# Kernel tuning notes

Measured on AMD Instinct MI355X. Metric: run time of the kernel, lower is better.

Reference implementation:

```python
import jax, jax.numpy as jnp
import numpy as np

N = 50000      # nodes
E = 1_600_000  # edges
IN, H, H2, OUT = 256, 128, 64, 2
EPS = 1e-5     # BatchNorm eps


def setup_inputs() -> dict:
    key = jax.random.key(0)
    ks = jax.random.split(key, 18)
    inp = {
        "x": jax.random.normal(ks[0], (N, IN), dtype=jnp.float32),
        "edge_index": jax.random.randint(ks[1], (2, E), 0, N, dtype=jnp.int64),
        # GCNConv 1
        "W1": jax.random.normal(ks[2], (IN, H), dtype=jnp.float32) / np.sqrt(IN),
        "b1": jnp.zeros((H,), dtype=jnp.float32),
        "g1": jnp.ones((H,), dtype=jnp.float32),
        "be1": jnp.zeros((H,), dtype=jnp.float32),
        "m1": jax.random.normal(ks[3], (H,), dtype=jnp.float32) * 0.1,
        "v1": jax.random.uniform(ks[4], (H,), dtype=jnp.float32, minval=0.5, maxval=1.5),
        # GCNConv 2
        "W2": jax.random.normal(ks[5], (H, H2), dtype=jnp.float32) / np.sqrt(H),
        "b2": jnp.zeros((H2,), dtype=jnp.float32),
        "g2": jnp.ones((H2,), dtype=jnp.float32),
        "be2": jnp.zeros((H2,), dtype=jnp.float32),
        "m2": jax.random.normal(ks[6], (H2,), dtype=jnp.float32) * 0.1,
        "v2": jax.random.uniform(ks[7], (H2,), dtype=jnp.float32, minval=0.5, maxval=1.5),
        # final linear
        "Wl": jax.random.normal(ks[8], (H2, OUT), dtype=jnp.float32) / np.sqrt(H2),
        "bl": jnp.zeros((OUT,), dtype=jnp.float32),
    }
    return inp


def _gcn_conv(x, W, b, src, dst, n_nodes):
    # PyG GCNConv: linear transform, then symmetric-normalized aggregation
    # with self-loops (gcn_norm, improved=False, fill_value=1).
    xw = x @ W                                            # [N, H]
    ones = jnp.ones((src.shape[0],), dtype=x.dtype)
    deg = jax.ops.segment_sum(ones, dst, num_segments=n_nodes) + 1.0  # +1 self-loop
    dinv = jax.lax.rsqrt(deg)                             # deg^{-1/2}
    norm = dinv[src] * dinv[dst]                          # [E]
    msgs = xw[src] * norm[:, None]                        # [E, H] gather
    agg = jax.ops.segment_sum(msgs, dst, num_segments=n_nodes)  # scatter-add
    agg = agg + xw * (1.0 / deg)[:, None]                 # self-loop term
    return agg + b


def _bn_relu(x, gamma, beta, mean, var):
    # inference-mode BatchNorm1d + ReLU
    xhat = (x - mean) * jax.lax.rsqrt(var + EPS)
    return jax.nn.relu(xhat * gamma + beta)


def reference(x, edge_index, W1, b1, g1, be1, m1, v1,
              W2, b2, g2, be2, m2, v2, Wl, bl):
    src, dst = edge_index[0], edge_index[1]
    h = _gcn_conv(x, W1, b1, src, dst, N)
    h = _bn_relu(h, g1, be1, m1, v1)
    # dropout is identity in eval mode
    h = _gcn_conv(h, W2, b2, src, dst, N)
    h = _bn_relu(h, g2, be2, m2, v2)
    return h @ Wl + bl
```

## Files before the change

### kernel.cpp

```cpp
#include <hip/hip_runtime.h>

#define N_NODES 50000
#define N_EDGES 1600000
#define IN_F 256
#define H1_F 128
#define H2_F 64
#define OUT_F 2
#define BN_EPS 1e-5f

#define NBUK 782
#define BCAP 3584
#define CHUNK 4096
#define NCHUNK 391

typedef __attribute__((ext_vector_type(8))) short bf16x8;
typedef __attribute__((ext_vector_type(4))) float f32x4;
typedef __attribute__((ext_vector_type(4))) int   i32x4;
typedef __attribute__((ext_vector_type(4))) unsigned u32x4;

__device__ __forceinline__ unsigned short f2b(float f) {
    union { float f; unsigned u; } v; v.f = f;
    unsigned r = (v.u + 0x7FFFu + ((v.u >> 16) & 1u)) >> 16;
    return (unsigned short)r;
}
__device__ __forceinline__ float b2f(unsigned short b) {
    union { unsigned u; float f; } v; v.u = ((unsigned)b) << 16;
    return v.f;
}
__device__ __forceinline__ void add2(float& a0, float& a1, unsigned u) {
    union { unsigned u; float f; } lo, hi;
    lo.u = u << 16;
    hi.u = u & 0xFFFF0000u;
    a0 += lo.f; a1 += hi.f;
}

__launch_bounds__(256)
__global__ void chist_prep_kernel(const int* __restrict__ dst, int* __restrict__ h,
                                  int* __restrict__ tot, int* __restrict__ deg,
                                  const float* __restrict__ W1, const float* __restrict__ W2,
                                  unsigned short* __restrict__ w1t, unsigned short* __restrict__ w2t,
                                  const float* __restrict__ g1, const float* __restrict__ be1,
                                  const float* __restrict__ m1, const float* __restrict__ v1,
                                  const float* __restrict__ b1,
                                  const float* __restrict__ g2, const float* __restrict__ be2,
                                  const float* __restrict__ m2, const float* __restrict__ v2,
                                  const float* __restrict__ b2,
                                  float* __restrict__ sc1, float* __restrict__ sh1,
                                  float* __restrict__ sc2, float* __restrict__ sh2) {
    const int blk = blockIdx.x;
    const int t   = threadIdx.x;
    if (blk < NCHUNK) {
        __shared__ int lh[NBUK];
        const int c = blk;
        for (int i = t; i < NBUK; i += 256) lh[i] = 0;
        __syncthreads();
        const int e0 = c * CHUNK;
        const int e1 = min(e0 + CHUNK, N_EDGES);
        const i32x4* p = (const i32x4*)(dst + e0);
        const int n4 = (e1 - e0) >> 2;
        for (int i = t; i < n4; i += 256) {
            i32x4 d = __builtin_nontemporal_load(p + i);
            atomicAdd(&lh[d.x >> 6], 1);
            atomicAdd(&lh[d.y >> 6], 1);
            atomicAdd(&lh[d.z >> 6], 1);
            atomicAdd(&lh[d.w >> 6], 1);
            atomicAdd(&deg[d.x], 1);
            atomicAdd(&deg[d.y], 1);
            atomicAdd(&deg[d.z], 1);
            atomicAdd(&deg[d.w], 1);
        }
        __syncthreads();
        for (int i = t; i < NBUK; i += 256) {
            int v = lh[i];
            h[(size_t)i * NCHUNK + c] = v;
            if (v) atomicAdd(&tot[i], v);
        }
    } else {
        const int blk2 = blk - NCHUNK;
        if (blk2 < 128) {
            int i = blk2 * 256 + t;
            int n = i / IN_F, k = i % IN_F;
            w1t[i] = f2b(W1[(size_t)k * H1_F + n]);
        } else if (blk2 < 160) {
            int i = (blk2 - 128) * 256 + t;
            int n = i / H1_F, k = i % H1_F;
            w2t[i] = f2b(W2[(size_t)k * H2_F + n]);
        } else {
            if (t < H1_F) {
                float s = g1[t] * rsqrtf(v1[t] + BN_EPS);
                sc1[t] = s;
                sh1[t] = (b1[t] - m1[t]) * s + be1[t];
            } else if (t < H1_F + H2_F) {
                int f = t - H1_F;
                float s = g2[f] * rsqrtf(v2[f] + BN_EPS);
                sc2[f] = s;
                sh2[f] = (b2[f] - m2[f]) * s + be2[f];
            }
        }
    }
}

__launch_bounds__(256)
__global__ void scanoffs_kernel(const int* __restrict__ tot, int* __restrict__ boff,
                                int* __restrict__ h, int* __restrict__ rowptr,
                                const int* __restrict__ deg, float* __restrict__ dinv) {
    const int b = (blockIdx.x * blockDim.x + threadIdx.x) >> 6;
    if (b >= NBUK) return;
    const int lane = threadIdx.x & 63;

    const int node = b * 64 + lane;
    if (node < N_NODES) dinv[node] = rsqrtf((float)deg[node] + 1.0f);

    int acc = 0;
    for (int i = lane; i < NBUK; i += 64)
        if (i < b) acc += tot[i];
#pragma unroll
    for (int off = 1; off < 64; off <<= 1) acc += __shfl_xor(acc, off);
    if (lane == 0) boff[b] = acc;
    if (b == 0 && lane == 0) { boff[NBUK] = N_EDGES; rowptr[N_NODES] = N_EDGES; }

    int run = acc;
    int* row = h + (size_t)b * NCHUNK;
    for (int c0 = 0; c0 < NCHUNK; c0 += 64) {
        int idx = c0 + lane;
        int v = (idx < NCHUNK) ? row[idx] : 0;
        int s = v;
#pragma unroll
        for (int off = 1; off < 64; off <<= 1) {
            int t2 = __shfl_up(s, off);
            if (lane >= off) s += t2;
        }
        if (idx < NCHUNK) row[idx] = run + (s - v);
        run += __shfl(s, 63);
    }
}

__launch_bounds__(256)
__global__ void cscatter_gemm1_kernel(const int* __restrict__ src, const int* __restrict__ dst,
                                      const int* __restrict__ h, unsigned* __restrict__ bedges,
                                      const float* __restrict__ x, const unsigned short* __restrict__ BT,
                                      const float* __restrict__ dinv, unsigned short* __restrict__ C) {
    __shared__ int cur[NBUK];
    const int blk = blockIdx.x;
    if (blk < NCHUNK) {
        const int c = blk;
        for (int i = threadIdx.x; i < NBUK; i += 256) cur[i] = h[(size_t)i * NCHUNK + c];
        __syncthreads();
        const int e0 = c * CHUNK;
        const int e1 = min(e0 + CHUNK, N_EDGES);
        const i32x4* pd = (const i32x4*)(dst + e0);
        const i32x4* ps = (const i32x4*)(src + e0);
        const int n4 = (e1 - e0) >> 2;
        for (int i = threadIdx.x; i < n4; i += 256) {
            i32x4 d = __builtin_nontemporal_load(pd + i);
            i32x4 s = __builtin_nontemporal_load(ps + i);
            int slot;
            slot = atomicAdd(&cur[d.x >> 6], 1); bedges[slot] = (unsigned)s.x | ((unsigned)d.x << 16);
            slot = atomicAdd(&cur[d.y >> 6], 1); bedges[slot] = (unsigned)s.y | ((unsigned)d.y << 16);
            slot = atomicAdd(&cur[d.z >> 6], 1); bedges[slot] = (unsigned)s.z | ((unsigned)d.z << 16);
            slot = atomicAdd(&cur[d.w >> 6], 1); bedges[slot] = (unsigned)s.w | ((unsigned)d.w << 16);
        }
    } else {
        constexpr int KSTEPS = IN_F / 32;
        constexpr int NTILES = H1_F / 16;
        constexpr int K  = IN_F;
        constexpr int NF = H1_F;
        const int bid2 = blk - NCHUNK;
        const int wave = threadIdx.x >> 6;
        const int lane = threadIdx.x & 63;
        const int r0   = (bid2 * 4 + wave) * 16;
        const int m    = lane & 15;
        const int kb   = lane >> 4;

        int arow = r0 + m;
        if (arow >= N_NODES) arow = N_NODES - 1;

        f32x4 acc[NTILES];
#pragma unroll
        for (int nt = 0; nt < NTILES; ++nt) acc[nt] = (f32x4)(0.f);

#pragma unroll
        for (int ks = 0; ks < KSTEPS; ++ks) {
            const int k0 = ks * 32 + kb * 8;
            const float* af = x + (size_t)arow * K + k0;
            f32x4 lo = __builtin_nontemporal_load((const f32x4*)af);
            f32x4 hi = __builtin_nontemporal_load((const f32x4*)(af + 4));
            union { bf16x8 v; unsigned short u[8]; } pk;
            pk.u[0] = f2b(lo.x); pk.u[1] = f2b(lo.y); pk.u[2] = f2b(lo.z); pk.u[3] = f2b(lo.w);
            pk.u[4] = f2b(hi.x); pk.u[5] = f2b(hi.y); pk.u[6] = f2b(hi.z); pk.u[7] = f2b(hi.w);
            bf16x8 a = pk.v;
#pragma unroll
            for (int nt = 0; nt < NTILES; ++nt) {
                bf16x8 b = *(const bf16x8*)(BT + (size_t)(nt * 16 + m) * K + k0);
                acc[nt] = __builtin_amdgcn_mfma_f32_16x16x32_bf16(a, b, acc[nt], 0, 0, 0);
            }
        }

#pragma unroll
        for (int reg = 0; reg < 4; ++reg) {
            const int r = r0 + kb * 4 + reg;
            if (r < N_NODES) {
                const float ds = dinv[r];
#pragma unroll
                for (int nt = 0; nt < NTILES; ++nt)
                    C[(size_t)r * NF + nt * 16 + m] = f2b(acc[nt][reg] * ds);
            }
        }
    }
}

__launch_bounds__(256)
__global__ void build_kernel(const unsigned* __restrict__ bedges, const int* __restrict__ boff,
                             unsigned short* __restrict__ perm, int* __restrict__ rowptr) {
    __shared__ unsigned e_lds[BCAP];
    __shared__ unsigned short p_lds[BCAP];
    __shared__ int ncnt[64], ncur[64];

    const int b = blockIdx.x;
    const int t = threadIdx.x;
    const int start = boff[b];
    const int end   = boff[b + 1];
    const int cnt   = end - start;
    const bool fits = (cnt <= BCAP);

    if (t < 64) ncnt[t] = 0;
    __syncthreads();

    for (int i = t; i < cnt; i += 256) {
        unsigned e = bedges[start + i];
        if (fits) e_lds[i] = e;
        atomicAdd(&ncnt[(e >> 16) & 63], 1);
    }
    __syncthreads();

    if (t == 0) {
        int a = 0;
        for (int i = 0; i < 64; ++i) { ncur[i] = a; a += ncnt[i]; }
    }
    __syncthreads();

    if (t < 64) {
        int node = b * 64 + t;
        if (node < N_NODES) rowptr[node] = start + ncur[t];
    }
    __syncthreads();

    for (int i = t; i < cnt; i += 256) {
        unsigned e = fits ? e_lds[i] : bedges[start + i];
        int slot = atomicAdd(&ncur[(e >> 16) & 63], 1);
        unsigned short s = (unsigned short)(e & 0xFFFFu);
        if (fits) p_lds[slot] = s;
        else      perm[start + slot] = s;
    }
    if (fits) {
        __syncthreads();
        for (int i = t; i < cnt; i += 256) perm[start + i] = p_lds[i];
    }
}

template <int KSTEPS, int NTILES>
__launch_bounds__(256)
__global__ void mfma_gemm2_kernel(const unsigned short* __restrict__ Ap, const unsigned short* __restrict__ BT,
                                  const float* __restrict__ dscale, unsigned short* __restrict__ C) {
    constexpr int K  = KSTEPS * 32;
    constexpr int NF = NTILES * 16;
    const int wave = threadIdx.x >> 6;
    const int lane = threadIdx.x & 63;
    const int r0   = (blockIdx.x * 4 + wave) * 16;
    const int m    = lane & 15;
    const int kb   = lane >> 4;

    int arow = r0 + m;
    if (arow >= N_NODES) arow = N_NODES - 1;

    f32x4 acc[NTILES];
#pragma unroll
    for (int nt = 0; nt < NTILES; ++nt) acc[nt] = (f32x4)(0.f);

#pragma unroll
    for (int ks = 0; ks < KSTEPS; ++ks) {
        const int k0 = ks * 32 + kb * 8;
        bf16x8 a = *(const bf16x8*)(Ap + (size_t)arow * K + k0);
#pragma unroll
        for (int nt = 0; nt < NTILES; ++nt) {
            bf16x8 b = *(const bf16x8*)(BT + (size_t)(nt * 16 + m) * K + k0);
            acc[nt] = __builtin_amdgcn_mfma_f32_16x16x32_bf16(a, b, acc[nt], 0, 0, 0);
        }
    }

#pragma unroll
    for (int reg = 0; reg < 4; ++reg) {
        const int r = r0 + kb * 4 + reg;
        if (r < N_NODES) {
            const float ds = dscale[r];
#pragma unroll
            for (int nt = 0; nt < NTILES; ++nt)
                C[(size_t)r * NF + nt * 16 + m] = f2b(acc[nt][reg] * ds);
        }
    }
}

template <int HF, bool FINAL>
__launch_bounds__(256)
__global__ void agg_kernel(const int* __restrict__ rowptr, const unsigned short* __restrict__ perm,
                           const unsigned short* __restrict__ xw, const float* __restrict__ dinv,
                           const float* __restrict__ sc, const float* __restrict__ sh,
                           const float* __restrict__ Wl, const float* __restrict__ bl,
                           void* __restrict__ outp) {
    constexpr int LPE = HF / 8;
    constexpr int G   = 64 / LPE;
    const int wave = threadIdx.x >> 6;
    const int node = blockIdx.x * 4 + wave;
    if (node >= N_NODES) return;
    const int lane = threadIdx.x & 63;
    const int grp  = lane / LPE;
    const int fl   = (lane % LPE) * 8;

    float aA[8];
#pragma unroll
    for (int i = 0; i < 8; ++i) aA[i] = 0.f;

    if (grp == 0) {
        u32x4 u = *(const u32x4*)(xw + (size_t)node * HF + fl);
#pragma unroll
        for (int i = 0; i < 4; ++i) add2(aA[2 * i], aA[2 * i + 1], u[i]);
    }

    const int start = rowptr[node];
    const int end   = rowptr[node + 1];
    for (int base = start; base < end; base += 64) {
        int pidx = base + lane;
        int pv = (int)__builtin_nontemporal_load(perm + (pidx < end ? pidx : end - 1));
        int ne = end - base;
        if (ne > 64) ne = 64;
        if (ne == 64) {
#pragma unroll
            for (int j = 0; j < 64; j += G) {
                int s = __shfl(pv, j + grp);
                u32x4 u = *(const u32x4*)(xw + (size_t)s * HF + fl);
#pragma unroll
                for (int i = 0; i < 4; ++i) add2(aA[2 * i], aA[2 * i + 1], u[i]);
            }
        } else {
            for (int j = 0; j < ne; j += G) {
                int s = __shfl(pv, j + grp);
                if (j + grp < ne) {
                    u32x4 u = *(const u32x4*)(xw + (size_t)s * HF + fl);
#pragma unroll
                    for (int i = 0; i < 4; ++i) add2(aA[2 * i], aA[2 * i + 1], u[i]);
                }
            }
        }
    }

#pragma unroll
    for (int off = LPE; off < 64; off <<= 1)
#pragma unroll
        for (int i = 0; i < 8; ++i) aA[i] += __shfl_xor(aA[i], off);

    const float dv = dinv[node];
    f32x4 scl = *(const f32x4*)(sc + fl);
    f32x4 sch = *(const f32x4*)(sc + fl + 4);
    f32x4 shl = *(const f32x4*)(sh + fl);
    f32x4 shh = *(const f32x4*)(sh + fl + 4);
    float y[8];
#pragma unroll
    for (int i = 0; i < 4; ++i) {
        y[i]     = fmaxf(aA[i] * (dv * scl[i]) + shl[i], 0.f);
        y[i + 4] = fmaxf(aA[i + 4] * (dv * sch[i]) + shh[i], 0.f);
    }

    if constexpr (!FINAL) {
        if (lane < LPE) {
            u32x4 o;
#pragma unroll
            for (int i = 0; i < 4; ++i)
                o[i] = (unsigned)f2b(y[2 * i]) | ((unsigned)f2b(y[2 * i + 1]) << 16);
            __builtin_nontemporal_store(o, (u32x4*)((unsigned short*)outp + (size_t)node * HF + fl));
        }
    } else {
        float p0 = 0.f, p1 = 0.f;
#pragma unroll
        for (int i = 0; i < 8; ++i) {
            p0 += y[i] * Wl[(fl + i) * 2 + 0];
            p1 += y[i] * Wl[(fl + i) * 2 + 1];
        }
#pragma unroll
        for (int off = 1; off < LPE; off <<= 1) {
            p0 += __shfl_xor(p0, off);
            p1 += __shfl_xor(p1, off);
        }
        if (lane == 0) {
            float* o = (float*)outp;
            o[(size_t)node * 2 + 0] = p0 + bl[0];
            o[(size_t)node * 2 + 1] = p1 + bl[1];
        }
    }
}

extern "C" void kernel_launch(void* const* d_in, const int* in_sizes, int n_in,
                              void* d_out, int out_size, void* d_ws, size_t ws_size,
                              hipStream_t stream) {
    const float* x   = (const float*)d_in[0];
    const int*   ei  = (const int*)d_in[1];
    const float* W1  = (const float*)d_in[2];
    const float* b1  = (const float*)d_in[3];
    const float* g1  = (const float*)d_in[4];
    const float* be1 = (const float*)d_in[5];
    const float* m1  = (const float*)d_in[6];
    const float* v1  = (const float*)d_in[7];
    const float* W2  = (const float*)d_in[8];
    const float* b2  = (const float*)d_in[9];
    const float* g2  = (const float*)d_in[10];
    const float* be2 = (const float*)d_in[11];
    const float* m2  = (const float*)d_in[12];
    const float* v2  = (const float*)d_in[13];
    const float* Wl  = (const float*)d_in[14];
    const float* bl  = (const float*)d_in[15];

    const int* src = ei;
    const int* dst = ei + N_EDGES;

    int*            h      = (int*)d_ws;
    int*            tot    = h + (size_t)NBUK * NCHUNK;
    int*            deg    = tot + 1024;
    int*            boff   = deg + 50048;
    int*            rowptr = boff + 1024;
    float*          dinv   = (float*)(rowptr + 50016);
    float*          sc1    = dinv + 50016;
    float*          sh1    = sc1 + 128;
    float*          sc2    = sh1 + 128;
    float*          sh2    = sc2 + 64;
    unsigned*       bedges = (unsigned*)(sh2 + 64);
    unsigned short* perm   = (unsigned short*)(bedges + N_EDGES);
    unsigned short* xwb    = perm + N_EDGES;
    unsigned short* h1b    = xwb + (size_t)N_NODES * H1_F;
    unsigned short* w1t    = h1b + (size_t)N_NODES * H1_F;
    unsigned short* w2t    = w1t + H1_F * IN_F;

    hipMemsetAsync(tot, 0, (1024 + 50048) * sizeof(int), stream);

    chist_prep_kernel<<<NCHUNK + 161, 256, 0, stream>>>(dst, h, tot, deg,
                                                        W1, W2, w1t, w2t,
                                                        g1, be1, m1, v1, b1,
                                                        g2, be2, m2, v2, b2,
                                                        sc1, sh1, sc2, sh2);
    scanoffs_kernel<<<(NBUK * 64 + 255) / 256, 256, 0, stream>>>(tot, boff, h, rowptr, deg, dinv);
    cscatter_gemm1_kernel<<<NCHUNK + (N_NODES + 63) / 64, 256, 0, stream>>>(
        src, dst, h, bedges, x, w1t, dinv, xwb);
    build_kernel<<<NBUK, 256, 0, stream>>>(bedges, boff, perm, rowptr);

    agg_kernel<H1_F, false><<<(N_NODES + 3) / 4, 256, 0, stream>>>(
        rowptr, perm, xwb, dinv, sc1, sh1, nullptr, nullptr, h1b);

    mfma_gemm2_kernel<H1_F / 32, H2_F / 16><<<(N_NODES + 63) / 64, 256, 0, stream>>>(
        h1b, w2t, dinv, xwb);
    agg_kernel<H2_F, true><<<(N_NODES + 3) / 4, 256, 0, stream>>>(
        rowptr, perm, xwb, dinv, sc2, sh2, Wl, bl, (float*)d_out);
}
```

Baseline: 299.8 us.

## Derive degrees from bucket build and apply source normalization during aggregation

Drops the 1.6M global per-node degree atomics from the histogram kernel. dinv is now computed from the per-node counts the build kernel already has in shared memory. Because dinv is no longer ready when the GEMMs run, the source-side scaling moves out of the GEMM epilogues and into the aggregation loop: each lane loads dinv[src] alongside perm and broadcasts it with a shuffle, then uses FMA instead of add. This adds one scattered dinv gather per edge per layer and shrinks the memset.

```diff
diff --git a/kernel.cpp b/kernel.cpp
--- a/kernel.cpp
+++ b/kernel.cpp
@@ -27,16 +27,17 @@
     union { unsigned u; float f; } v; v.u = ((unsigned)b) << 16;
     return v.f;
 }
-__device__ __forceinline__ void add2(float& a0, float& a1, unsigned u) {
+__device__ __forceinline__ void fma2(float& a0, float& a1, unsigned u, float s) {
     union { unsigned u; float f; } lo, hi;
     lo.u = u << 16;
     hi.u = u & 0xFFFF0000u;
-    a0 += lo.f; a1 += hi.f;
+    a0 += lo.f * s;
+    a1 += hi.f * s;
 }
 
 __launch_bounds__(256)
 __global__ void chist_prep_kernel(const int* __restrict__ dst, int* __restrict__ h,
-                                  int* __restrict__ tot, int* __restrict__ deg,
+                                  int* __restrict__ tot,
                                   const float* __restrict__ W1, const float* __restrict__ W2,
                                   unsigned short* __restrict__ w1t, unsigned short* __restrict__ w2t,
                                   const float* __restrict__ g1, const float* __restrict__ be1,
@@ -64,10 +65,6 @@
             atomicAdd(&lh[d.y >> 6], 1);
             atomicAdd(&lh[d.z >> 6], 1);
             atomicAdd(&lh[d.w >> 6], 1);
-            atomicAdd(&deg[d.x], 1);
-            atomicAdd(&deg[d.y], 1);
-            atomicAdd(&deg[d.z], 1);
-            atomicAdd(&deg[d.w], 1);
         }
         __syncthreads();
         for (int i = t; i < NBUK; i += 256) {
@@ -102,14 +99,10 @@
 
 __launch_bounds__(256)
 __global__ void scanoffs_kernel(const int* __restrict__ tot, int* __restrict__ boff,
-                                int* __restrict__ h, int* __restrict__ rowptr,
-                                const int* __restrict__ deg, float* __restrict__ dinv) {
+                                int* __restrict__ h, int* __restrict__ rowptr) {
     const int b = (blockIdx.x * blockDim.x + threadIdx.x) >> 6;
     if (b >= NBUK) return;
     const int lane = threadIdx.x & 63;
-
-    const int node = b * 64 + lane;
-    if (node < N_NODES) dinv[node] = rsqrtf((float)deg[node] + 1.0f);
 
     int acc = 0;
     for (int i = lane; i < NBUK; i += 64)
@@ -139,7 +132,7 @@
 __global__ void cscatter_gemm1_kernel(const int* __restrict__ src, const int* __restrict__ dst,
                                       const int* __restrict__ h, unsigned* __restrict__ bedges,
                                       const float* __restrict__ x, const unsigned short* __restrict__ BT,
-                                      const float* __restrict__ dinv, unsigned short* __restrict__ C) {
+                                      unsigned short* __restrict__ C) {
     __shared__ int cur[NBUK];
     const int blk = blockIdx.x;
     if (blk < NCHUNK) {
@@ -200,10 +193,9 @@
         for (int reg = 0; reg < 4; ++reg) {
             const int r = r0 + kb * 4 + reg;
             if (r < N_NODES) {
-                const float ds = dinv[r];
 #pragma unroll
                 for (int nt = 0; nt < NTILES; ++nt)
-                    C[(size_t)r * NF + nt * 16 + m] = f2b(acc[nt][reg] * ds);
+                    C[(size_t)r * NF + nt * 16 + m] = f2b(acc[nt][reg]);
             }
         }
     }
@@ -211,7 +203,8 @@
 
 __launch_bounds__(256)
 __global__ void build_kernel(const unsigned* __restrict__ bedges, const int* __restrict__ boff,
-                             unsigned short* __restrict__ perm, int* __restrict__ rowptr) {
+                             unsigned short* __restrict__ perm, int* __restrict__ rowptr,
+                             float* __restrict__ dinv) {
     __shared__ unsigned e_lds[BCAP];
     __shared__ unsigned short p_lds[BCAP];
     __shared__ int ncnt[64], ncur[64];
@@ -241,7 +234,10 @@
 
     if (t < 64) {
         int node = b * 64 + t;
-        if (node < N_NODES) rowptr[node] = start + ncur[t];
+        if (node < N_NODES) {
+            rowptr[node] = start + ncur[t];
+            dinv[node]   = rsqrtf((float)ncnt[t] + 1.0f);
+        }
     }
     __syncthreads();
 
@@ -261,7 +257,7 @@
 template <int KSTEPS, int NTILES>
 __launch_bounds__(256)
 __global__ void mfma_gemm2_kernel(const unsigned short* __restrict__ Ap, const unsigned short* __restrict__ BT,
-                                  const float* __restrict__ dscale, unsigned short* __restrict__ C) {
+                                  unsigned short* __restrict__ C) {
     constexpr int K  = KSTEPS * 32;
     constexpr int NF = NTILES * 16;
     const int wave = threadIdx.x >> 6;
@@ -292,10 +288,9 @@
     for (int reg = 0; reg < 4; ++reg) {
         const int r = r0 + kb * 4 + reg;
         if (r < N_NODES) {
-            const float ds = dscale[r];
 #pragma unroll
             for (int nt = 0; nt < NTILES; ++nt)
-                C[(size_t)r * NF + nt * 16 + m] = f2b(acc[nt][reg] * ds);
+                C[(size_t)r * NF + nt * 16 + m] = f2b(acc[nt][reg]);
         }
     }
 }
@@ -316,6 +311,8 @@
     const int grp  = lane / LPE;
     const int fl   = (lane % LPE) * 8;
 
+    const float dv = dinv[node];
+
     float aA[8];
 #pragma unroll
     for (int i = 0; i < 8; ++i) aA[i] = 0.f;
@@ -323,7 +320,7 @@
     if (grp == 0) {
         u32x4 u = *(const u32x4*)(xw + (size_t)node * HF + fl);
 #pragma unroll
-        for (int i = 0; i < 4; ++i) add2(aA[2 * i], aA[2 * i + 1], u[i]);
+        for (int i = 0; i < 4; ++i) fma2(aA[2 * i], aA[2 * i + 1], u[i], dv);
     }
 
     const int start = rowptr[node];
@@ -331,23 +328,26 @@
     for (int base = start; base < end; base += 64) {
         int pidx = base + lane;
         int pv = (int)__builtin_nontemporal_load(perm + (pidx < end ? pidx : end - 1));
+        float dvs = dinv[pv];
         int ne = end - base;
         if (ne > 64) ne = 64;
         if (ne == 64) {
 #pragma unroll
             for (int j = 0; j < 64; j += G) {
-                int s = __shfl(pv, j + grp);
+                int s    = __shfl(pv, j + grp);
+                float dd = __shfl(dvs, j + grp);
                 u32x4 u = *(const u32x4*)(xw + (size_t)s * HF + fl);
 #pragma unroll
-                for (int i = 0; i < 4; ++i) add2(aA[2 * i], aA[2 * i + 1], u[i]);
+                for (int i = 0; i < 4; ++i) fma2(aA[2 * i], aA[2 * i + 1], u[i], dd);
             }
         } else {
             for (int j = 0; j < ne; j += G) {
-                int s = __shfl(pv, j + grp);
+                int s    = __shfl(pv, j + grp);
+                float dd = __shfl(dvs, j + grp);
                 if (j + grp < ne) {
                     u32x4 u = *(const u32x4*)(xw + (size_t)s * HF + fl);
 #pragma unroll
-                    for (int i = 0; i < 4; ++i) add2(aA[2 * i], aA[2 * i + 1], u[i]);
+                    for (int i = 0; i < 4; ++i) fma2(aA[2 * i], aA[2 * i + 1], u[i], dd);
                 }
             }
         }
@@ -358,7 +358,6 @@
 #pragma unroll
         for (int i = 0; i < 8; ++i) aA[i] += __shfl_xor(aA[i], off);
 
-    const float dv = dinv[node];
     f32x4 scl = *(const f32x4*)(sc + fl);
     f32x4 sch = *(const f32x4*)(sc + fl + 4);
     f32x4 shl = *(const f32x4*)(sh + fl);
@@ -423,8 +422,7 @@
 
     int*            h      = (int*)d_ws;
     int*            tot    = h + (size_t)NBUK * NCHUNK;
-    int*            deg    = tot + 1024;
-    int*            boff   = deg + 50048;
+    int*            boff   = tot + 1024;
     int*            rowptr = boff + 1024;
     float*          dinv   = (float*)(rowptr + 50016);
     float*          sc1    = dinv + 50016;
@@ -438,23 +436,23 @@
     unsigned short* w1t    = h1b + (size_t)N_NODES * H1_F;
     unsigned short* w2t    = w1t + H1_F * IN_F;
 
-    hipMemsetAsync(tot, 0, (1024 + 50048) * sizeof(int), stream);
-
-    chist_prep_kernel<<<NCHUNK + 161, 256, 0, stream>>>(dst, h, tot, deg,
+    hipMemsetAsync(tot, 0, 1024 * sizeof(int), stream);
+
+    chist_prep_kernel<<<NCHUNK + 161, 256, 0, stream>>>(dst, h, tot,
                                                         W1, W2, w1t, w2t,
                                                         g1, be1, m1, v1, b1,
                                                         g2, be2, m2, v2, b2,
                                                         sc1, sh1, sc2, sh2);
-    scanoffs_kernel<<<(NBUK * 64 + 255) / 256, 256, 0, stream>>>(tot, boff, h, rowptr, deg, dinv);
+    scanoffs_kernel<<<(NBUK * 64 + 255) / 256, 256, 0, stream>>>(tot, boff, h, rowptr);
     cscatter_gemm1_kernel<<<NCHUNK + (N_NODES + 63) / 64, 256, 0, stream>>>(
-        src, dst, h, bedges, x, w1t, dinv, xwb);
-    build_kernel<<<NBUK, 256, 0, stream>>>(bedges, boff, perm, rowptr);
+        src, dst, h, bedges, x, w1t, xwb);
+    build_kernel<<<NBUK, 256, 0, stream>>>(bedges, boff, perm, rowptr, dinv);
 
     agg_kernel<H1_F, false><<<(N_NODES + 3) / 4, 256, 0, stream>>>(
         rowptr, perm, xwb, dinv, sc1, sh1, nullptr, nullptr, h1b);
 
     mfma_gemm2_kernel<H1_F / 32, H2_F / 16><<<(N_NODES + 63) / 64, 256, 0, stream>>>(
-        h1b, w2t, dinv, xwb);
+        h1b, w2t, xwb);
     agg_kernel<H2_F, true><<<(N_NODES + 3) / 4, 256, 0, stream>>>(
         rowptr, perm, xwb, dinv, sc2, sh2, Wl, bl, (float*)d_out);
 }
```

Result: faster. 261.4 us (-12.8%).
